# Optimization experiments

Measured on AMD Instinct MI355X. Metric: run time of the kernel, lower is better.

Reference implementation:

```python
import jax, jax.numpy as jnp
import numpy as np

N_TOK, EMBED, N_CLS, BATCH, N_HEAD = 32768, 512, 16, 8, 8
D_HEAD = EMBED // N_HEAD


def setup_inputs() -> dict:
    key0 = jax.random.key(0)
    ks = jax.random.split(key0, 12)
    s = 1.0 / np.sqrt(EMBED)
    query = jax.random.normal(ks[0], (N_TOK, EMBED), dtype=jnp.float32)
    key_f = jax.random.normal(ks[1], (N_CLS, BATCH, EMBED), dtype=jnp.float32)
    val_f = jax.random.normal(ks[2], (N_CLS, BATCH, EMBED), dtype=jnp.float32)
    batch_idx = jnp.sort(jax.random.randint(ks[3], (N_TOK,), 0, BATCH)).astype(jnp.int32)
    Wq = jax.random.normal(ks[4], (EMBED, EMBED), dtype=jnp.float32) * s
    bq = jnp.zeros((EMBED,), dtype=jnp.float32)
    Wk = jax.random.normal(ks[5], (EMBED, EMBED), dtype=jnp.float32) * s  # Conv1d(k=1) kernel squeezed
    bk = jnp.zeros((EMBED,), dtype=jnp.float32)
    Wv = jax.random.normal(ks[6], (EMBED, EMBED), dtype=jnp.float32) * s
    bv = jnp.zeros((EMBED,), dtype=jnp.float32)
    Wo = jax.random.normal(ks[7], (EMBED, EMBED), dtype=jnp.float32) * s
    bo = jnp.zeros((EMBED,), dtype=jnp.float32)
    return {"query": query, "key": key_f, "value": val_f, "batch_idx": batch_idx,
            "batch_size": BATCH, "Wq": Wq, "bq": bq, "Wk": Wk, "bk": bk,
            "Wv": Wv, "bv": bv, "Wo": Wo, "bo": bo}


def reference(query, key, value, batch_idx, batch_size, Wq, bq, Wk, bk, Wv, bv, Wo, bo):
    n_tok, embed = query.shape
    L, B, _ = key.shape
    H, D = N_HEAD, EMBED // N_HEAD
    scale = D ** -0.5  # matmul_norm
    # projections (Conv1d with kernel_size=1 == pointwise linear over E)
    q = (query @ Wq.T + bq).reshape(n_tok, H, D)                           # [N,H,D]
    k = (jnp.einsum('lbe,fe->blf', key, Wk) + bk)                          # [B,L,E]
    k = k.transpose(0, 2, 1).reshape(B, H, D, L)                           # [B,H,D,L]
    v = (jnp.einsum('lbe,fe->blf', value, Wv) + bv)                        # [B,L,E]
    v = v.transpose(0, 2, 1).reshape(B, H, D, L).transpose(0, 1, 3, 2)     # [B,H,L,D]
    # scores against every batch's prototypes, then pick each token's batch
    scores_all = jnp.einsum('nhd,bhdl->nbhl', q, k) * scale                # [N,B,H,L]
    sel = batch_idx.astype(jnp.int32)[:, None, None, None]
    scores = jnp.take_along_axis(scores_all, sel, axis=1).squeeze(1)       # [N,H,L]
    p = jax.nn.softmax(scores, axis=-1)
    ctx_all = jnp.einsum('nhl,bhld->nbhd', p, v)                           # [N,B,H,D]
    ctx = jnp.take_along_axis(ctx_all, sel, axis=1).squeeze(1)             # [N,H,D]
    return ctx.reshape(n_tok, embed) @ Wo.T + bo
```

## Files before the change

### kernel.cpp

```cpp
#include <hip/hip_runtime.h>

typedef unsigned short u16;
typedef __attribute__((ext_vector_type(8))) short short8;
typedef __attribute__((ext_vector_type(4))) unsigned short u16x4;
typedef __attribute__((ext_vector_type(4))) float f32x4;

#define N_TOKENS 32768
#define EMBED 512
#define NCLS 16
#define NBATCH 8
#define NHEAD 8
#define DHEAD 64

__device__ __forceinline__ u16 f2bf(float f) {
  unsigned u = __float_as_uint(f);
  u += 0x7fffu + ((u >> 16) & 1u);
  return (u16)(u >> 16);
}

__device__ __forceinline__ void async16(const u16* g, u16* l) {
  __builtin_amdgcn_global_load_lds(
      (__attribute__((address_space(1))) const unsigned int*)(const void*)g,
      (__attribute__((address_space(3))) unsigned int*)(void*)l,
      16, 0, 0);
}

__global__ __launch_bounds__(256) void kvproj_kernel(
    const float* __restrict__ key, const float* __restrict__ val,
    const float* __restrict__ Wk, const float* __restrict__ bk,
    const float* __restrict__ Wv, const float* __restrict__ bv,
    float* __restrict__ kproj, float* __restrict__ vproj) {
  const int blk = blockIdx.x;
  const bool isV = blk & 1;
  const int b = (blk >> 1) & 7;
  const int l = (blk >> 4) & 15;
  const int fg = blk >> 8;
  const int wave = threadIdx.x >> 6;
  const int lane = threadIdx.x & 63;
  const int fbase = fg * 64 + wave * 16;
  const float* x = (isV ? val : key) + ((size_t)l * NBATCH + b) * EMBED;
  const float* W = isV ? Wv : Wk;
  const float* bias = isV ? bv : bk;

  float4 x0 = *(const float4*)(x + lane * 8);
  float4 x1 = *(const float4*)(x + lane * 8 + 4);

#pragma unroll
  for (int grp = 0; grp < 4; grp++) {
    float acc[4];
#pragma unroll
    for (int j = 0; j < 4; j++) {
      const float* w = W + (size_t)(fbase + grp * 4 + j) * EMBED + lane * 8;
      float4 w0 = *(const float4*)w;
      float4 w1 = *(const float4*)(w + 4);
      acc[j] = x0.x * w0.x + x0.y * w0.y + x0.z * w0.z + x0.w * w0.w +
               x1.x * w1.x + x1.y * w1.y + x1.z * w1.z + x1.w * w1.w;
    }
#pragma unroll
    for (int j = 0; j < 4; j++) {
      acc[j] += __shfl_xor(acc[j], 1);
      acc[j] += __shfl_xor(acc[j], 2);
      acc[j] += __shfl_xor(acc[j], 4);
      acc[j] += __shfl_xor(acc[j], 8);
      acc[j] += __shfl_xor(acc[j], 16);
      acc[j] += __shfl_xor(acc[j], 32);
    }
#pragma unroll
    for (int j = 0; j < 4; j++) {
      if (lane == j) {
        const int f = fbase + grp * 4 + j;
        float v = acc[j] + bias[f];
        if (!isV) {
          kproj[((size_t)(b * EMBED + f)) * NCLS + l] = v;
        } else {
          vproj[(size_t)b * 8192 + (size_t)(f >> 6) * 1024 + l * 64 + (f & 63)] = v;
        }
      }
    }
  }
}

__global__ __launch_bounds__(256) void build_all(
    const float* __restrict__ kproj, const float* __restrict__ vproj,
    const float* __restrict__ Wq, const float* __restrict__ bq,
    const float* __restrict__ Wo,
    u16* __restrict__ Kqb, u16* __restrict__ WoVb, float* __restrict__ sb) {
  const int blk = blockIdx.x;
  if (blk < 2048) {
    int t = blk * 256 + threadIdx.x;
    int e = t & 511;
    int hl = (t >> 9) & 127;
    int b = t >> 16;
    int h = hl >> 4, l = hl & 15;
    const float* kp = kproj + (size_t)b * 8192 + h * 1024 + l;
    const float* wq = Wq + (size_t)(h * 64) * 512 + e;
    float acc = 0.f;
#pragma unroll 16
    for (int d = 0; d < 64; d++) acc += kp[d * 16] * wq[d * 512];
    Kqb[t] = f2bf(acc);
  } else if (blk < 3072) {
    const int wave = threadIdx.x >> 6;
    const int lane = threadIdx.x & 63;
    const int wgid = (blk - 2048) * 4 + wave;
    const int b = wgid >> 9, f = wgid & 511;
    const int l = lane >> 2, c = lane & 3;
    const float* vp = vproj + (size_t)b * 8192 + l * 64 + c * 16;
    const float* wo = Wo + (size_t)f * 512 + c * 16;
#pragma unroll 2
    for (int h = 0; h < 8; h++) {
      const float* v = vp + h * 1024;
      const float* w = wo + h * 64;
      float4 v0 = *(const float4*)v,       w0 = *(const float4*)w;
      float4 v1 = *(const float4*)(v + 4), w1 = *(const float4*)(w + 4);
      float4 v2 = *(const float4*)(v + 8), w2 = *(const float4*)(w + 8);
      float4 v3 = *(const float4*)(v + 12), w3 = *(const float4*)(w + 12);
      float acc = v0.x * w0.x + v0.y * w0.y + v0.z * w0.z + v0.w * w0.w +
                  v1.x * w1.x + v1.y * w1.y + v1.z * w1.z + v1.w * w1.w +
                  v2.x * w2.x + v2.y * w2.y + v2.z * w2.z + v2.w * w2.w +
                  v3.x * w3.x + v3.y * w3.y + v3.z * w3.z + v3.w * w3.w;
      acc += __shfl_xor(acc, 1);
      acc += __shfl_xor(acc, 2);
      if (c == 0) WoVb[(size_t)b * 65536 + (size_t)f * 128 + h * 16 + l] = f2bf(acc);
    }
  } else {
    int t = (blk - 3072) * 256 + threadIdx.x;
    int hl = t & 127, b = t >> 7;
    int h = hl >> 4, l = hl & 15;
    const float* kp = kproj + (size_t)b * 8192 + h * 1024 + l;
    const float* q = bq + h * 64;
    float acc = 0.f;
#pragma unroll
    for (int d = 0; d < 64; d++) acc += q[d] * kp[d * 16];
    sb[t] = acc;
  }
}

__global__ __launch_bounds__(256) void fused_attn(
    const float* __restrict__ query, const u16* __restrict__ Kqb,
    const u16* __restrict__ WoVb, const float* __restrict__ sb,
    const float* __restrict__ bo, const int* __restrict__ bidx,
    float* __restrict__ out) {
  __shared__ __align__(16) u16 Bs[2][128 * 64];
  __shared__ __align__(16) u16 Ps[64 * 128];
  const int tid = threadIdx.x;
  const int lane = tid & 63;
  const int wave = tid >> 6;
  const int quad = lane >> 4;
  const int l16 = lane & 15;
  const int tileId = blockIdx.x & 511;
  const int slot = blockIdx.x >> 9;
  const int m0 = tileId * 64;
  const int bFirst = bidx[m0];
  const int bLast = bidx[m0 + 63];
  if (slot == 1 && bFirst == bLast) return;
  const int b0 = (slot == 0) ? bFirst : bFirst + 1;
  const int b1 = (slot == 0) ? bFirst : bLast;

  const int rB = tid >> 3;
  const int lgB = (tid & 7) ^ (rB & 7);
  const size_t bbase = (size_t)rB * 512 + lgB * 8;

  int rowb[4][4];
#pragma unroll
  for (int mi = 0; mi < 4; mi++)
#pragma unroll
    for (int r = 0; r < 4; r++) rowb[mi][r] = bidx[m0 + mi * 16 + quad * 4 + r];

  const float* pA = query + (size_t)(m0 + wave * 16 + l16) * 512 + quad * 8;

  for (int bb = b0; bb <= b1; bb++) {
    const u16* Bq = Kqb + (size_t)bb * 65536;

#pragma unroll
    for (int i = 0; i < 4; i++)
      async16(Bq + bbase + (size_t)i * 32 * 512, &Bs[0][(tid + i * 256) * 8]);
    float4 aC[4];
    aC[0] = *(const float4*)(pA);
    aC[1] = *(const float4*)(pA + 4);
    aC[2] = *(const float4*)(pA + 32);
    aC[3] = *(const float4*)(pA + 36);

    f32x4 acc1[8];
#pragma unroll
    for (int j = 0; j < 8; j++) acc1[j] = (f32x4){0.f, 0.f, 0.f, 0.f};

    for (int t = 0; t < 8; t++) {
      __syncthreads();
      const int cur = t & 1;
      if (t < 7) {
        const size_t ko = (size_t)(t + 1) * 64;
#pragma unroll
        for (int i = 0; i < 4; i++)
          async16(Bq + bbase + ko + (size_t)i * 32 * 512, &Bs[cur ^ 1][(tid + i * 256) * 8]);
      }
      float4 a0 = aC[0], a1 = aC[1], a2 = aC[2], a3 = aC[3];
      if (t < 7) {
        const float* p = pA + (t + 1) * 64;
        aC[0] = *(const float4*)(p);
        aC[1] = *(const float4*)(p + 4);
        aC[2] = *(const float4*)(p + 32);
        aC[3] = *(const float4*)(p + 36);
      }
      short8 af[2];
      af[0][0] = (short)f2bf(a0.x); af[0][1] = (short)f2bf(a0.y);
      af[0][2] = (short)f2bf(a0.z); af[0][3] = (short)f2bf(a0.w);
      af[0][4] = (short)f2bf(a1.x); af[0][5] = (short)f2bf(a1.y);
      af[0][6] = (short)f2bf(a1.z); af[0][7] = (short)f2bf(a1.w);
      af[1][0] = (short)f2bf(a2.x); af[1][1] = (short)f2bf(a2.y);
      af[1][2] = (short)f2bf(a2.z); af[1][3] = (short)f2bf(a2.w);
      af[1][4] = (short)f2bf(a3.x); af[1][5] = (short)f2bf(a3.y);
      af[1][6] = (short)f2bf(a3.z); af[1][7] = (short)f2bf(a3.w);
      __builtin_amdgcn_s_setprio(1);
#pragma unroll
      for (int kk = 0; kk < 2; kk++) {
#pragma unroll
        for (int ni = 0; ni < 8; ni++) {
          const int rw = ni * 16 + l16;
          const int phys = (kk * 4 + quad) ^ (rw & 7);
          short8 bfr = *(const short8*)&Bs[cur][rw * 64 + phys * 8];
          acc1[ni] = __builtin_amdgcn_mfma_f32_16x16x32_bf16(af[kk], bfr, acc1[ni], 0, 0, 0);
        }
      }
      __builtin_amdgcn_s_setprio(0);
    }

    float sbv[8];
#pragma unroll
    for (int ni = 0; ni < 8; ni++) sbv[ni] = sb[bb * 128 + ni * 16 + l16];
#pragma unroll
    for (int r = 0; r < 4; r++) {
      const int row = wave * 16 + quad * 4 + r;
#pragma unroll
      for (int ni = 0; ni < 8; ni++) {
        float v = acc1[ni][r] + sbv[ni];
        float mx = v;
        mx = fmaxf(mx, __shfl_xor(mx, 1));
        mx = fmaxf(mx, __shfl_xor(mx, 2));
        mx = fmaxf(mx, __shfl_xor(mx, 4));
        mx = fmaxf(mx, __shfl_xor(mx, 8));
        float ev = __expf((v - mx) * 0.125f);
        float s = ev;
        s += __shfl_xor(s, 1);
        s += __shfl_xor(s, 2);
        s += __shfl_xor(s, 4);
        s += __shfl_xor(s, 8);
        const int col = ni * 16 + l16;
        Ps[row * 128 + (((col >> 3) ^ (row & 7)) << 3) + (col & 7)] = f2bf(ev / s);
      }
    }
    __syncthreads();

    const u16* Wv = WoVb + (size_t)bb * 65536;
#pragma unroll
    for (int h2 = 0; h2 < 2; h2++) {
      const int f0 = wave * 128 + h2 * 64;
      f32x4 acc2[4][4];
#pragma unroll
      for (int i = 0; i < 4; i++)
#pragma unroll
        for (int j = 0; j < 4; j++) acc2[i][j] = (f32x4){0.f, 0.f, 0.f, 0.f};
#pragma unroll
      for (int kk = 0; kk < 4; kk++) {
        short8 paf[4], bf2[4];
#pragma unroll
        for (int mi = 0; mi < 4; mi++) {
          const int row = mi * 16 + l16;
          paf[mi] = *(const short8*)&Ps[row * 128 + (((kk * 4 + quad) ^ (row & 7)) << 3)];
        }
#pragma unroll
        for (int ni = 0; ni < 4; ni++) {
          const int fr = f0 + ni * 16 + l16;
          bf2[ni] = *(const short8*)(Wv + (size_t)fr * 128 + kk * 32 + quad * 8);
        }
        __builtin_amdgcn_s_setprio(1);
#pragma unroll
        for (int mi = 0; mi < 4; mi++)
#pragma unroll
          for (int ni = 0; ni < 4; ni++)
            acc2[mi][ni] = __builtin_amdgcn_mfma_f32_16x16x32_bf16(paf[mi], bf2[ni], acc2[mi][ni], 0, 0, 0);
        __builtin_amdgcn_s_setprio(0);
      }
      float bov[4];
#pragma unroll
      for (int ni = 0; ni < 4; ni++) bov[ni] = bo[f0 + ni * 16 + l16];
#pragma unroll
      for (int mi = 0; mi < 4; mi++)
#pragma unroll
        for (int r = 0; r < 4; r++) {
          if (rowb[mi][r] == bb) {
            const size_t row = m0 + mi * 16 + quad * 4 + r;
#pragma unroll
            for (int ni = 0; ni < 4; ni++)
              out[row * 512 + f0 + ni * 16 + l16] = acc2[mi][ni][r] + bov[ni];
          }
        }
    }
    __syncthreads();
  }
}

extern "C" void kernel_launch(void* const* d_in, const int* in_sizes, int n_in,
                              void* d_out, int out_size, void* d_ws, size_t ws_size,
                              hipStream_t stream) {
  const float* query = (const float*)d_in[0];
  const float* keyt = (const float*)d_in[1];
  const float* valt = (const float*)d_in[2];
  const int* bidx = (const int*)d_in[3];
  const float* Wq = (const float*)d_in[5];
  const float* bq = (const float*)d_in[6];
  const float* Wk = (const float*)d_in[7];
  const float* bk = (const float*)d_in[8];
  const float* Wv = (const float*)d_in[9];
  const float* bv = (const float*)d_in[10];
  const float* Wo = (const float*)d_in[11];
  const float* bo = (const float*)d_in[12];
  float* out = (float*)d_out;

  unsigned char* w = (unsigned char*)d_ws;
  float* kproj = (float*)(w + 41943040ull);
  float* vproj = (float*)(w + 42205184ull);
  u16* Kqb = (u16*)(w + 42467328ull);
  u16* WoVb = (u16*)(w + 43515904ull);
  float* sb = (float*)(w + 44564480ull);

  kvproj_kernel<<<2048, 256, 0, stream>>>(keyt, valt, Wk, bk, Wv, bv, kproj, vproj);

  build_all<<<3076, 256, 0, stream>>>(kproj, vproj, Wq, bq, Wo, Kqb, WoVb, sb);

  fused_attn<<<N_TOKENS / 64 * 2, 256, 0, stream>>>(query, Kqb, WoVb, sb, bo, bidx, out);
}
```

Before: 223.6 us.

## Shrink LDS K-tile, split output GEMM accumulators, drop softmax max pass

```diff
diff --git a/kernel.cpp b/kernel.cpp
--- a/kernel.cpp
+++ b/kernel.cpp
@@ -140,7 +140,7 @@
     const u16* __restrict__ WoVb, const float* __restrict__ sb,
     const float* __restrict__ bo, const int* __restrict__ bidx,
     float* __restrict__ out) {
-  __shared__ __align__(16) u16 Bs[2][128 * 64];
+  __shared__ __align__(16) u16 Bs[2][128 * 32];
   __shared__ __align__(16) u16 Ps[64 * 128];
   const int tid = threadIdx.x;
   const int lane = tid & 63;
@@ -156,70 +156,50 @@
   const int b0 = (slot == 0) ? bFirst : bFirst + 1;
   const int b1 = (slot == 0) ? bFirst : bLast;
 
-  const int rB = tid >> 3;
-  const int lgB = (tid & 7) ^ (rB & 7);
-  const size_t bbase = (size_t)rB * 512 + lgB * 8;
-
-  int rowb[4][4];
-#pragma unroll
-  for (int mi = 0; mi < 4; mi++)
-#pragma unroll
-    for (int r = 0; r < 4; r++) rowb[mi][r] = bidx[m0 + mi * 16 + quad * 4 + r];
+  const int r0 = tid >> 2, r1 = r0 + 64;
+  const int lg0 = (tid & 3) ^ ((r0 >> 1) & 3);
+  const int lg1 = (tid & 3) ^ ((r1 >> 1) & 3);
+  const size_t boff0 = (size_t)r0 * 512 + lg0 * 8;
+  const size_t boff1 = (size_t)r1 * 512 + lg1 * 8;
 
   const float* pA = query + (size_t)(m0 + wave * 16 + l16) * 512 + quad * 8;
 
   for (int bb = b0; bb <= b1; bb++) {
     const u16* Bq = Kqb + (size_t)bb * 65536;
 
-#pragma unroll
-    for (int i = 0; i < 4; i++)
-      async16(Bq + bbase + (size_t)i * 32 * 512, &Bs[0][(tid + i * 256) * 8]);
-    float4 aC[4];
-    aC[0] = *(const float4*)(pA);
-    aC[1] = *(const float4*)(pA + 4);
-    aC[2] = *(const float4*)(pA + 32);
-    aC[3] = *(const float4*)(pA + 36);
+    async16(Bq + boff0, &Bs[0][tid * 8]);
+    async16(Bq + boff1, &Bs[0][tid * 8 + 2048]);
+    float4 a0c = *(const float4*)(pA);
+    float4 a1c = *(const float4*)(pA + 4);
 
     f32x4 acc1[8];
 #pragma unroll
     for (int j = 0; j < 8; j++) acc1[j] = (f32x4){0.f, 0.f, 0.f, 0.f};
 
-    for (int t = 0; t < 8; t++) {
+    for (int t = 0; t < 16; t++) {
       __syncthreads();
       const int cur = t & 1;
-      if (t < 7) {
-        const size_t ko = (size_t)(t + 1) * 64;
-#pragma unroll
-        for (int i = 0; i < 4; i++)
-          async16(Bq + bbase + ko + (size_t)i * 32 * 512, &Bs[cur ^ 1][(tid + i * 256) * 8]);
-      }
-      float4 a0 = aC[0], a1 = aC[1], a2 = aC[2], a3 = aC[3];
-      if (t < 7) {
-        const float* p = pA + (t + 1) * 64;
-        aC[0] = *(const float4*)(p);
-        aC[1] = *(const float4*)(p + 4);
-        aC[2] = *(const float4*)(p + 32);
-        aC[3] = *(const float4*)(p + 36);
-      }
-      short8 af[2];
-      af[0][0] = (short)f2bf(a0.x); af[0][1] = (short)f2bf(a0.y);
-      af[0][2] = (short)f2bf(a0.z); af[0][3] = (short)f2bf(a0.w);
-      af[0][4] = (short)f2bf(a1.x); af[0][5] = (short)f2bf(a1.y);
-      af[0][6] = (short)f2bf(a1.z); af[0][7] = (short)f2bf(a1.w);
-      af[1][0] = (short)f2bf(a2.x); af[1][1] = (short)f2bf(a2.y);
-      af[1][2] = (short)f2bf(a2.z); af[1][3] = (short)f2bf(a2.w);
-      af[1][4] = (short)f2bf(a3.x); af[1][5] = (short)f2bf(a3.y);
-      af[1][6] = (short)f2bf(a3.z); af[1][7] = (short)f2bf(a3.w);
+      if (t < 15) {
+        const int ko = (t + 1) * 32;
+        async16(Bq + boff0 + ko, &Bs[cur ^ 1][tid * 8]);
+        async16(Bq + boff1 + ko, &Bs[cur ^ 1][tid * 8 + 2048]);
+      }
+      float4 a0 = a0c, a1 = a1c;
+      if (t < 15) {
+        a0c = *(const float4*)(pA + (t + 1) * 32);
+        a1c = *(const float4*)(pA + (t + 1) * 32 + 4);
+      }
+      short8 af;
+      af[0] = (short)f2bf(a0.x); af[1] = (short)f2bf(a0.y);
+      af[2] = (short)f2bf(a0.z); af[3] = (short)f2bf(a0.w);
+      af[4] = (short)f2bf(a1.x); af[5] = (short)f2bf(a1.y);
+      af[6] = (short)f2bf(a1.z); af[7] = (short)f2bf(a1.w);
       __builtin_amdgcn_s_setprio(1);
 #pragma unroll
-      for (int kk = 0; kk < 2; kk++) {
-#pragma unroll
-        for (int ni = 0; ni < 8; ni++) {
-          const int rw = ni * 16 + l16;
-          const int phys = (kk * 4 + quad) ^ (rw & 7);
-          short8 bfr = *(const short8*)&Bs[cur][rw * 64 + phys * 8];
-          acc1[ni] = __builtin_amdgcn_mfma_f32_16x16x32_bf16(af[kk], bfr, acc1[ni], 0, 0, 0);
-        }
+      for (int ni = 0; ni < 8; ni++) {
+        const int rw = ni * 16 + l16;
+        short8 bfr = *(const short8*)&Bs[cur][rw * 32 + ((quad ^ ((rw >> 1) & 3)) << 3)];
+        acc1[ni] = __builtin_amdgcn_mfma_f32_16x16x32_bf16(af, bfr, acc1[ni], 0, 0, 0);
       }
       __builtin_amdgcn_s_setprio(0);
     }
@@ -233,12 +213,7 @@
 #pragma unroll
       for (int ni = 0; ni < 8; ni++) {
         float v = acc1[ni][r] + sbv[ni];
-        float mx = v;
-        mx = fmaxf(mx, __shfl_xor(mx, 1));
-        mx = fmaxf(mx, __shfl_xor(mx, 2));
-        mx = fmaxf(mx, __shfl_xor(mx, 4));
-        mx = fmaxf(mx, __shfl_xor(mx, 8));
-        float ev = __expf((v - mx) * 0.125f);
+        float ev = __expf(v * 0.125f);
         float s = ev;
         s += __shfl_xor(s, 1);
         s += __shfl_xor(s, 2);
@@ -253,47 +228,51 @@
     const u16* Wv = WoVb + (size_t)bb * 65536;
 #pragma unroll
     for (int h2 = 0; h2 < 2; h2++) {
-      const int f0 = wave * 128 + h2 * 64;
-      f32x4 acc2[4][4];
-#pragma unroll
-      for (int i = 0; i < 4; i++)
-#pragma unroll
-        for (int j = 0; j < 4; j++) acc2[i][j] = (f32x4){0.f, 0.f, 0.f, 0.f};
-#pragma unroll
-      for (int kk = 0; kk < 4; kk++) {
-        short8 paf[4], bf2[4];
-#pragma unroll
-        for (int mi = 0; mi < 4; mi++) {
-          const int row = mi * 16 + l16;
-          paf[mi] = *(const short8*)&Ps[row * 128 + (((kk * 4 + quad) ^ (row & 7)) << 3)];
+#pragma unroll
+      for (int nh = 0; nh < 2; nh++) {
+        const int f0 = wave * 128 + h2 * 64 + nh * 32;
+        f32x4 acc2[4][2];
+#pragma unroll
+        for (int i = 0; i < 4; i++)
+#pragma unroll
+          for (int j = 0; j < 2; j++) acc2[i][j] = (f32x4){0.f, 0.f, 0.f, 0.f};
+#pragma unroll
+        for (int kk = 0; kk < 4; kk++) {
+          short8 paf[4], bf2[2];
+#pragma unroll
+          for (int mi = 0; mi < 4; mi++) {
+            const int row = mi * 16 + l16;
+            paf[mi] = *(const short8*)&Ps[row * 128 + (((kk * 4 + quad) ^ (row & 7)) << 3)];
+          }
+#pragma unroll
+          for (int nj = 0; nj < 2; nj++) {
+            const int fr = f0 + nj * 16 + l16;
+            bf2[nj] = *(const short8*)(Wv + (size_t)fr * 128 + kk * 32 + quad * 8);
+          }
+          __builtin_amdgcn_s_setprio(1);
+#pragma unroll
+          for (int mi = 0; mi < 4; mi++)
+#pragma unroll
+            for (int nj = 0; nj < 2; nj++)
+              acc2[mi][nj] = __builtin_amdgcn_mfma_f32_16x16x32_bf16(paf[mi], bf2[nj], acc2[mi][nj], 0, 0, 0);
+          __builtin_amdgcn_s_setprio(0);
         }
-#pragma unroll
-        for (int ni = 0; ni < 4; ni++) {
-          const int fr = f0 + ni * 16 + l16;
-          bf2[ni] = *(const short8*)(Wv + (size_t)fr * 128 + kk * 32 + quad * 8);
-        }
-        __builtin_amdgcn_s_setprio(1);
+        float bov[2];
+#pragma unroll
+        for (int nj = 0; nj < 2; nj++) bov[nj] = bo[f0 + nj * 16 + l16];
 #pragma unroll
         for (int mi = 0; mi < 4; mi++)
 #pragma unroll
-          for (int ni = 0; ni < 4; ni++)
-            acc2[mi][ni] = __builtin_amdgcn_mfma_f32_16x16x32_bf16(paf[mi], bf2[ni], acc2[mi][ni], 0, 0, 0);
-        __builtin_amdgcn_s_setprio(0);
-      }
-      float bov[4];
-#pragma unroll
-      for (int ni = 0; ni < 4; ni++) bov[ni] = bo[f0 + ni * 16 + l16];
-#pragma unroll
-      for (int mi = 0; mi < 4; mi++)
-#pragma unroll
-        for (int r = 0; r < 4; r++) {
-          if (rowb[mi][r] == bb) {
-            const size_t row = m0 + mi * 16 + quad * 4 + r;
-#pragma unroll
-            for (int ni = 0; ni < 4; ni++)
-              out[row * 512 + f0 + ni * 16 + l16] = acc2[mi][ni][r] + bov[ni];
+          for (int r = 0; r < 4; r++) {
+            const int rb = bidx[m0 + mi * 16 + quad * 4 + r];
+            if (rb == bb) {
+              const size_t row = m0 + mi * 16 + quad * 4 + r;
+#pragma unroll
+              for (int nj = 0; nj < 2; nj++)
+                out[row * 512 + f0 + nj * 16 + l16] = acc2[mi][nj][r] + bov[nj];
+            }
           }
-        }
+      }
     }
     __syncthreads();
   }
```

After: 236.1 us. 5.6% more time.
